# Kernel optimization log

Measured on AMD Instinct MI355X. Metric: run time of the kernel, lower is better.

Reference implementation:

```python
import jax, jax.numpy as jnp
import numpy as np
import math
from jax import lax

L = 16
T = 2 ** 14          # hash table size (power of 2 -> uint32 arithmetic is exact mod T)
F_DIM = 2
N_MIN, N_MAX = 16, 512
_B = math.exp((math.log(N_MAX) - math.log(N_MIN)) / (L - 1))
NS = [int(N_MIN * _B ** i) for i in range(L)]
PRIME = np.uint32(2654435761)


def setup_inputs() -> dict:
    key = jax.random.key(0)
    k1, k2 = jax.random.split(key)
    x = jax.random.uniform(k1, (8, 2, 512, 512), dtype=jnp.float32)
    hash_table = jax.random.uniform(k2, (L, T, F_DIM), dtype=jnp.float32) * 2e-4 - 1e-4
    return {"x": x, "hash_table": hash_table}


def reference(x, hash_table):
    b, c, h, w = x.shape
    feats = []
    for i, n in enumerate(NS):
        kh, kw = h // n, w // n
        # max_pool2d(x*n, (kh,kw), stride=1) -> [b, 2, h-kh+1, w-kw+1]
        g = lax.reduce_window(x * n, -jnp.inf, lax.max,
                              (1, 1, kh, kw), (1, 1, 1, 1), 'VALID')
        g = g.astype(jnp.uint32)  # trunc toward zero, values nonneg and small
        # prime-XOR hash; T is a power of two so uint32 wraparound matches int64 math mod T
        idx = (g[:, 0] ^ (g[:, 1] * PRIME)) % np.uint32(T)  # [b, gh, gw]
        f = hash_table[i][idx]                 # gather -> [b, gh, gw, F_DIM]
        f = jnp.transpose(f, (0, 3, 1, 2))     # [b, F_DIM, gh, gw]
        # bilinear upsample (half-pixel centers == align_corners=False)
        f = jax.image.resize(f, (b, F_DIM, h, w), method='bilinear')
        feats.append(f)
    return jnp.concatenate(feats, axis=1)       # [b, L*F_DIM, h, w]
```

## Files before the change

kernel.cpp:

```cpp
#include <hip/hip_runtime.h>
#include <stdint.h>

#define NLVL 16
#define TSIZE 16384
#define HW 512

typedef float vfloat4 __attribute__((ext_vector_type(4)));

__constant__ int c_n[NLVL] = {16,20,25,32,40,50,64,80,101,128,161,203,256,322,406,512};

__device__ __forceinline__ uint32_t pkmax(uint32_t a, uint32_t b) {
    uint32_t r;
    asm("v_pk_max_u16 %0, %1, %2" : "=v"(r) : "v"(a), "v"(b));
    return r;
}

template<int K>
__device__ __forceinline__ void do_tile(
        const int lvl, const int b, const int tx0, const int ty0,
        const float* __restrict__ x, const float* __restrict__ table,
        float* __restrict__ out, uint32_t* lds) {
    constexpr int gh = 513 - K;
    constexpr float s = (float)gh * (1.0f / 512.0f);
    const float nf = (float)c_n[lvl];
    const int tid = threadIdx.x;

    const float* xb0 = x + (size_t)b * 2 * HW * HW;
    const float* xb1 = xb0 + HW * HW;
    const float2* tb = (const float2*)table + (size_t)lvl * TSIZE;
    float* ob = out + ((size_t)b * 32 + lvl * 2) * HW * HW;

    if constexpr (K == 1) {
        const int oy = tid >> 3, xo = tx0 + (tid & 7) * 4;
        const int y = ty0 + oy;
        const float4 v0 = *(const float4*)&xb0[y * HW + xo];
        const float4 v1 = *(const float4*)&xb1[y * HW + xo];
        vfloat4 o0, o1;
        {
            const uint32_t i0 = (((uint32_t)(v0.x * nf)) ^ (((uint32_t)(v1.x * nf)) * 2654435761u)) & (TSIZE - 1);
            const uint32_t i1 = (((uint32_t)(v0.y * nf)) ^ (((uint32_t)(v1.y * nf)) * 2654435761u)) & (TSIZE - 1);
            const uint32_t i2 = (((uint32_t)(v0.z * nf)) ^ (((uint32_t)(v1.z * nf)) * 2654435761u)) & (TSIZE - 1);
            const uint32_t i3 = (((uint32_t)(v0.w * nf)) ^ (((uint32_t)(v1.w * nf)) * 2654435761u)) & (TSIZE - 1);
            const float2 f0 = tb[i0], f1 = tb[i1], f2 = tb[i2], f3 = tb[i3];
            o0 = (vfloat4){f0.x, f1.x, f2.x, f3.x};
            o1 = (vfloat4){f0.y, f1.y, f2.y, f3.y};
        }
        const size_t o = (size_t)y * HW + xo;
        __builtin_nontemporal_store(o0, (vfloat4*)&ob[o]);
        __builtin_nontemporal_store(o1, (vfloat4*)&ob[o + (size_t)HW * HW]);
        return;
    }

    uint32_t* V   = lds;
    float2*  feat = (float2*)(lds + 33 * 68);

    const int gy_base = (int)floorf(((float)ty0 + 0.5f) * s - 0.5f);
    const int gx_base = (int)floorf(((float)tx0 + 0.5f) * s - 0.5f);
    const int rmin = max(gy_base, 0);
    const int cmin = max(gx_base, 0);

    {
        const int wv = __builtin_amdgcn_readfirstlane(tid >> 6);
        const int c  = tid & 63;
        const int r0 = 8 * wv;
        const int xx = min(cmin + c, HW - 1);
        const int ybase = rmin + r0;
        uint32_t e[K + 8];
#pragma unroll
        for (int t = 0; t < K + 8; ++t) {
            const int yy = min(ybase + t, HW - 1);
            const float* rp0 = xb0 + yy * HW;
            const float* rp1 = xb1 + yy * HW;
            const float v0 = rp0[xx];
            const float v1 = rp1[xx];
            e[t] = (uint32_t)(v0 * nf) | ((uint32_t)(v1 * nf) << 16);
        }
        uint32_t o[9];
        if constexpr (K >= 10) {
            uint32_t sfx[9];
            sfx[8] = e[8];
#pragma unroll
            for (int t = 7; t >= 0; --t) sfx[t] = pkmax(e[t], sfx[t + 1]);
            uint32_t run = e[9];
#pragma unroll
            for (int m = 9; m <= K + 7; ++m) {
                if (m > 9) run = pkmax(run, e[m]);
                if (m >= K - 1) o[m - K + 1] = pkmax(sfx[m - K + 1], run);
            }
        } else {
#pragma unroll
            for (int i = 0; i < 9; ++i) {
                uint32_t m = e[i];
#pragma unroll
                for (int t = 1; t < K; ++t) m = pkmax(m, e[i + t]);
                o[i] = m;
            }
        }
        const int vb = r0 * 68 + c;
#pragma unroll
        for (int t = 0; t < 9; ++t) V[vb + t * 68] = o[t];
    }
    __syncthreads();

    if (tid < 99) {
        const int i = tid / 3, g = tid % 3;
        constexpr int NE  = 12 + K - 1;
        constexpr int NCH = (NE + 3) >> 2;
        uint32_t f[NCH * 4];
        const uint4* rp = (const uint4*)(V + i * 68 + 12 * g);
#pragma unroll
        for (int cc = 0; cc < NCH; ++cc) {
            const uint4 q = rp[cc];
            f[4*cc] = q.x; f[4*cc+1] = q.y; f[4*cc+2] = q.z; f[4*cc+3] = q.w;
        }
        uint32_t wm[12];
        if constexpr (K >= 13) {
            uint32_t sfx[12];
            sfx[11] = f[11];
#pragma unroll
            for (int d = 10; d >= 0; --d) sfx[d] = pkmax(f[d], sfx[d + 1]);
            uint32_t run = f[12];
#pragma unroll
            for (int m = 12; m <= K + 10; ++m) {
                if (m > 12) run = pkmax(run, f[m]);
                if (m >= K - 1) wm[m - K + 1] = pkmax(sfx[m - K + 1], run);
            }
        } else {
#pragma unroll
            for (int d = 0; d < 12; ++d) {
                uint32_t m = f[d];
#pragma unroll
                for (int t = 1; t < K; ++t) m = pkmax(m, f[d + t]);
                wm[d] = m;
            }
        }
#pragma unroll
        for (int d = 0; d < 12; ++d) {
            const int j = 12 * g + d;
            if (j < 33) {
                const uint32_t m = wm[d];
                const uint32_t idx = ((m & 0xFFFFu) ^ ((m >> 16) * 2654435761u)) & (TSIZE - 1);
                feat[i * 34 + j] = tb[idx];
            }
        }
    }
    __syncthreads();

    const int bty = tid >> 5, btx = tid & 31;
    const int xo = tx0 + btx;
    const float sxf = ((float)xo + 0.5f) * s - 0.5f;
    const float fxf = floorf(sxf);
    const float wx = sxf - fxf;
    const int x0i = (int)fxf;
    const int jx0 = min(max(x0i, 0), gh - 1) - cmin;
    const int jx1 = min(max(x0i + 1, 0), gh - 1) - cmin;
    for (int oy = bty; oy < 32; oy += 8) {
        const int y = ty0 + oy;
        const float syf = ((float)y + 0.5f) * s - 0.5f;
        const float fyf = floorf(syf);
        const float wy = syf - fyf;
        const int y0i = (int)fyf;
        const int iy0 = min(max(y0i, 0), gh - 1) - rmin;
        const int iy1 = min(max(y0i + 1, 0), gh - 1) - rmin;
        const float2 f00 = feat[iy0 * 34 + jx0], f01 = feat[iy0 * 34 + jx1];
        const float2 f10 = feat[iy1 * 34 + jx0], f11 = feat[iy1 * 34 + jx1];
        const float w11 = wy * wx;
        const float w10 = wy - w11;
        const float w01 = wx - w11;
        const float w00 = 1.0f - wy - wx + w11;
        const float c0 = f00.x * w00 + f01.x * w01 + f10.x * w10 + f11.x * w11;
        const float c1 = f00.y * w00 + f01.y * w01 + f10.y * w10 + f11.y * w11;
        const size_t o = (size_t)y * HW + xo;
        __builtin_nontemporal_store(c0, &ob[o]);
        __builtin_nontemporal_store(c1, &ob[o + (size_t)HW * HW]);
    }
}

__global__ __launch_bounds__(256) void fused_kernel(
        const float* __restrict__ x, const float* __restrict__ table,
        float* __restrict__ out) {
    __shared__ __align__(16) uint32_t lds[33 * 68 + 33 * 34 * 2];

    const int bid  = blockIdx.x;
    const int b    = bid & 7;
    const int tile = (bid >> 3) & 255;
    const int lvl  = bid >> 11;
    const int tx0  = (tile & 15) * 32;
    const int ty0  = (tile >> 4) * 32;

    switch (lvl) {
        case  0: do_tile<32>( 0, b, tx0, ty0, x, table, out, lds); break;
        case  1: do_tile<25>( 1, b, tx0, ty0, x, table, out, lds); break;
        case  2: do_tile<20>( 2, b, tx0, ty0, x, table, out, lds); break;
        case  3: do_tile<16>( 3, b, tx0, ty0, x, table, out, lds); break;
        case  4: do_tile<12>( 4, b, tx0, ty0, x, table, out, lds); break;
        case  5: do_tile<10>( 5, b, tx0, ty0, x, table, out, lds); break;
        case  6: do_tile< 8>( 6, b, tx0, ty0, x, table, out, lds); break;
        case  7: do_tile< 6>( 7, b, tx0, ty0, x, table, out, lds); break;
        case  8: do_tile< 5>( 8, b, tx0, ty0, x, table, out, lds); break;
        case  9: do_tile< 4>( 9, b, tx0, ty0, x, table, out, lds); break;
        case 10: do_tile< 3>(10, b, tx0, ty0, x, table, out, lds); break;
        case 11: do_tile< 2>(11, b, tx0, ty0, x, table, out, lds); break;
        case 12: do_tile< 2>(12, b, tx0, ty0, x, table, out, lds); break;
        case 13: do_tile< 1>(13, b, tx0, ty0, x, table, out, lds); break;
        case 14: do_tile< 1>(14, b, tx0, ty0, x, table, out, lds); break;
        default: do_tile< 1>(15, b, tx0, ty0, x, table, out, lds); break;
    }
}

extern "C" void kernel_launch(void* const* d_in, const int* in_sizes, int n_in,
                              void* d_out, int out_size, void* d_ws, size_t ws_size,
                              hipStream_t stream) {
    const float* x     = (const float*)d_in[0];
    const float* table = (const float*)d_in[1];
    float* out         = (float*)d_out;
    (void)d_ws; (void)ws_size;

    fused_kernel<<<dim3(NLVL * 256 * 8), dim3(256), 0, stream>>>(x, table, out);
}
```

Baseline: 111.3 us.

## Widen tiles to 64 columns with two-pixel-per-thread processing

Output tiles grow from 32x32 to 32x64, which halves the block count. Each thread now handles two adjacent columns: it reads x with float2 loads, runs packed max pooling on two columns, and writes two outputs per row with vector stores. The larger tile shrinks the relative halo overhead in the separable max-pool and gives wider memory transactions. In exchange it uses more LDS and registers per block, which can lower occupancy for the large-K levels, and there are half as many blocks to spread across the GPU.

```diff
diff --git a/kernel.cpp b/kernel.cpp
--- a/kernel.cpp
+++ b/kernel.cpp
@@ -6,6 +6,7 @@
 #define HW 512
 
 typedef float vfloat4 __attribute__((ext_vector_type(4)));
+typedef float vfloat2 __attribute__((ext_vector_type(2)));
 
 __constant__ int c_n[NLVL] = {16,20,25,32,40,50,64,80,101,128,161,203,256,322,406,512};
 
@@ -31,83 +32,89 @@
     float* ob = out + ((size_t)b * 32 + lvl * 2) * HW * HW;
 
     if constexpr (K == 1) {
-        const int oy = tid >> 3, xo = tx0 + (tid & 7) * 4;
-        const int y = ty0 + oy;
-        const float4 v0 = *(const float4*)&xb0[y * HW + xo];
-        const float4 v1 = *(const float4*)&xb1[y * HW + xo];
-        vfloat4 o0, o1;
-        {
+        const int r = tid >> 4, cq = tid & 15;
+        const int xo = tx0 + cq * 4;
+#pragma unroll
+        for (int it = 0; it < 2; ++it) {
+            const int y = ty0 + r + it * 16;
+            const float4 v0 = *(const float4*)&xb0[y * HW + xo];
+            const float4 v1 = *(const float4*)&xb1[y * HW + xo];
             const uint32_t i0 = (((uint32_t)(v0.x * nf)) ^ (((uint32_t)(v1.x * nf)) * 2654435761u)) & (TSIZE - 1);
             const uint32_t i1 = (((uint32_t)(v0.y * nf)) ^ (((uint32_t)(v1.y * nf)) * 2654435761u)) & (TSIZE - 1);
             const uint32_t i2 = (((uint32_t)(v0.z * nf)) ^ (((uint32_t)(v1.z * nf)) * 2654435761u)) & (TSIZE - 1);
             const uint32_t i3 = (((uint32_t)(v0.w * nf)) ^ (((uint32_t)(v1.w * nf)) * 2654435761u)) & (TSIZE - 1);
             const float2 f0 = tb[i0], f1 = tb[i1], f2 = tb[i2], f3 = tb[i3];
-            o0 = (vfloat4){f0.x, f1.x, f2.x, f3.x};
-            o1 = (vfloat4){f0.y, f1.y, f2.y, f3.y};
-        }
-        const size_t o = (size_t)y * HW + xo;
-        __builtin_nontemporal_store(o0, (vfloat4*)&ob[o]);
-        __builtin_nontemporal_store(o1, (vfloat4*)&ob[o + (size_t)HW * HW]);
+            const vfloat4 o0 = (vfloat4){f0.x, f1.x, f2.x, f3.x};
+            const vfloat4 o1 = (vfloat4){f0.y, f1.y, f2.y, f3.y};
+            const size_t o = (size_t)y * HW + xo;
+            __builtin_nontemporal_store(o0, (vfloat4*)&ob[o]);
+            __builtin_nontemporal_store(o1, (vfloat4*)&ob[o + (size_t)HW * HW]);
+        }
         return;
     }
 
     uint32_t* V   = lds;
-    float2*  feat = (float2*)(lds + 33 * 68);
+    float2*  feat = (float2*)(lds + 33 * 108);
 
     const int gy_base = (int)floorf(((float)ty0 + 0.5f) * s - 0.5f);
     const int gx_base = (int)floorf(((float)tx0 + 0.5f) * s - 0.5f);
-    const int rmin = max(gy_base, 0);
-    const int cmin = max(gx_base, 0);
-
+    const int rmin  = max(gy_base, 0);
+    const int cmin  = max(gx_base, 0);
+    const int xbase = cmin & ~1;
+
+    constexpr int NEEDC = 66 + K - 1;
+    constexpr int LANES = (NEEDC + 1) / 2;
     {
         const int wv = __builtin_amdgcn_readfirstlane(tid >> 6);
-        const int c  = tid & 63;
-        const int r0 = 8 * wv;
-        const int xx = min(cmin + c, HW - 1);
-        const int ybase = rmin + r0;
-        uint32_t e[K + 8];
-#pragma unroll
-        for (int t = 0; t < K + 8; ++t) {
-            const int yy = min(ybase + t, HW - 1);
-            const float* rp0 = xb0 + yy * HW;
-            const float* rp1 = xb1 + yy * HW;
-            const float v0 = rp0[xx];
-            const float v1 = rp1[xx];
-            e[t] = (uint32_t)(v0 * nf) | ((uint32_t)(v1 * nf) << 16);
-        }
-        uint32_t o[9];
-        if constexpr (K >= 10) {
-            uint32_t sfx[9];
-            sfx[8] = e[8];
-#pragma unroll
-            for (int t = 7; t >= 0; --t) sfx[t] = pkmax(e[t], sfx[t + 1]);
-            uint32_t run = e[9];
-#pragma unroll
-            for (int m = 9; m <= K + 7; ++m) {
-                if (m > 9) run = pkmax(run, e[m]);
-                if (m >= K - 1) o[m - K + 1] = pkmax(sfx[m - K + 1], run);
-            }
-        } else {
-#pragma unroll
-            for (int i = 0; i < 9; ++i) {
-                uint32_t m = e[i];
-#pragma unroll
-                for (int t = 1; t < K; ++t) m = pkmax(m, e[i + t]);
-                o[i] = m;
-            }
-        }
-        const int vb = r0 * 68 + c;
-#pragma unroll
-        for (int t = 0; t < 9; ++t) V[vb + t * 68] = o[t];
+        const int l  = tid & 63;
+        if (l < LANES) {
+            const int r0 = 8 * wv;
+            const int xx = min(xbase + 2 * l, HW - 2);
+            const int ybase = rmin + r0;
+            uint32_t eA[K + 8], eB[K + 8];
+#pragma unroll
+            for (int t = 0; t < K + 8; ++t) {
+                const int yy = min(ybase + t, HW - 1);
+                const float2 v0 = *(const float2*)(xb0 + yy * HW + xx);
+                const float2 v1 = *(const float2*)(xb1 + yy * HW + xx);
+                eA[t] = (uint32_t)(v0.x * nf) | ((uint32_t)(v1.x * nf) << 16);
+                eB[t] = (uint32_t)(v0.y * nf) | ((uint32_t)(v1.y * nf) << 16);
+            }
+            uint32_t oA[9], oB[9];
+            if constexpr (K >= 10) {
+                uint32_t sA[9], sB[9];
+                sA[8] = eA[8]; sB[8] = eB[8];
+#pragma unroll
+                for (int t = 7; t >= 0; --t) { sA[t] = pkmax(eA[t], sA[t+1]); sB[t] = pkmax(eB[t], sB[t+1]); }
+                uint32_t rA = eA[9], rB = eB[9];
+#pragma unroll
+                for (int m = 9; m <= K + 7; ++m) {
+                    if (m > 9) { rA = pkmax(rA, eA[m]); rB = pkmax(rB, eB[m]); }
+                    if (m >= K - 1) { oA[m-K+1] = pkmax(sA[m-K+1], rA); oB[m-K+1] = pkmax(sB[m-K+1], rB); }
+                }
+            } else {
+#pragma unroll
+                for (int i = 0; i < 9; ++i) {
+                    uint32_t mA = eA[i], mB = eB[i];
+#pragma unroll
+                    for (int t = 1; t < K; ++t) { mA = pkmax(mA, eA[i+t]); mB = pkmax(mB, eB[i+t]); }
+                    oA[i] = mA; oB[i] = mB;
+                }
+            }
+            const int vb = r0 * 108 + 2 * l;
+#pragma unroll
+            for (int t = 0; t < 9; ++t)
+                *(uint2*)(V + vb + t * 108) = make_uint2(oA[t], oB[t]);
+        }
     }
     __syncthreads();
 
-    if (tid < 99) {
-        const int i = tid / 3, g = tid % 3;
+    if (tid < 198) {
+        const int i = tid / 6, g = tid % 6;
         constexpr int NE  = 12 + K - 1;
         constexpr int NCH = (NE + 3) >> 2;
         uint32_t f[NCH * 4];
-        const uint4* rp = (const uint4*)(V + i * 68 + 12 * g);
+        const uint4* rp = (const uint4*)(V + i * 108 + 12 * g);
 #pragma unroll
         for (int cc = 0; cc < NCH; ++cc) {
             const uint4 q = rp[cc];
@@ -136,24 +143,30 @@
         }
 #pragma unroll
         for (int d = 0; d < 12; ++d) {
-            const int j = 12 * g + d;
-            if (j < 33) {
+            const int p = 12 * g + d;
+            if (p < 66) {
                 const uint32_t m = wm[d];
                 const uint32_t idx = ((m & 0xFFFFu) ^ ((m >> 16) * 2654435761u)) & (TSIZE - 1);
-                feat[i * 34 + j] = tb[idx];
+                feat[i * 68 + p] = tb[idx];
             }
         }
     }
     __syncthreads();
 
     const int bty = tid >> 5, btx = tid & 31;
-    const int xo = tx0 + btx;
-    const float sxf = ((float)xo + 0.5f) * s - 0.5f;
-    const float fxf = floorf(sxf);
-    const float wx = sxf - fxf;
-    const int x0i = (int)fxf;
-    const int jx0 = min(max(x0i, 0), gh - 1) - cmin;
-    const int jx1 = min(max(x0i + 1, 0), gh - 1) - cmin;
+    const int xo = tx0 + 2 * btx;
+    const float sxA = ((float)xo + 0.5f) * s - 0.5f;
+    const float fxA = floorf(sxA);
+    const float wxA = sxA - fxA;
+    const int xiA = (int)fxA;
+    const int jA0 = min(max(xiA, 0), gh - 1) - xbase;
+    const int jA1 = min(max(xiA + 1, 0), gh - 1) - xbase;
+    const float sxB = ((float)xo + 1.5f) * s - 0.5f;
+    const float fxB = floorf(sxB);
+    const float wxB = sxB - fxB;
+    const int xiB = (int)fxB;
+    const int jB0 = min(max(xiB, 0), gh - 1) - xbase;
+    const int jB1 = min(max(xiB + 1, 0), gh - 1) - xbase;
     for (int oy = bty; oy < 32; oy += 8) {
         const int y = ty0 + oy;
         const float syf = ((float)y + 0.5f) * s - 0.5f;
@@ -162,31 +175,33 @@
         const int y0i = (int)fyf;
         const int iy0 = min(max(y0i, 0), gh - 1) - rmin;
         const int iy1 = min(max(y0i + 1, 0), gh - 1) - rmin;
-        const float2 f00 = feat[iy0 * 34 + jx0], f01 = feat[iy0 * 34 + jx1];
-        const float2 f10 = feat[iy1 * 34 + jx0], f11 = feat[iy1 * 34 + jx1];
-        const float w11 = wy * wx;
-        const float w10 = wy - w11;
-        const float w01 = wx - w11;
-        const float w00 = 1.0f - wy - wx + w11;
-        const float c0 = f00.x * w00 + f01.x * w01 + f10.x * w10 + f11.x * w11;
-        const float c1 = f00.y * w00 + f01.y * w01 + f10.y * w10 + f11.y * w11;
+        const float2* r0f = feat + iy0 * 68;
+        const float2* r1f = feat + iy1 * 68;
+        const float2 a00 = r0f[jA0], a01 = r0f[jA1], a10 = r1f[jA0], a11 = r1f[jA1];
+        const float wA11 = wy * wxA, wA10 = wy - wA11, wA01 = wxA - wA11, wA00 = 1.0f - wy - wxA + wA11;
+        const float cA0 = a00.x * wA00 + a01.x * wA01 + a10.x * wA10 + a11.x * wA11;
+        const float cA1 = a00.y * wA00 + a01.y * wA01 + a10.y * wA10 + a11.y * wA11;
+        const float2 b00 = r0f[jB0], b01 = r0f[jB1], b10 = r1f[jB0], b11 = r1f[jB1];
+        const float wB11 = wy * wxB, wB10 = wy - wB11, wB01 = wxB - wB11, wB00 = 1.0f - wy - wxB + wB11;
+        const float cB0 = b00.x * wB00 + b01.x * wB01 + b10.x * wB10 + b11.x * wB11;
+        const float cB1 = b00.y * wB00 + b01.y * wB01 + b10.y * wB10 + b11.y * wB11;
         const size_t o = (size_t)y * HW + xo;
-        __builtin_nontemporal_store(c0, &ob[o]);
-        __builtin_nontemporal_store(c1, &ob[o + (size_t)HW * HW]);
+        __builtin_nontemporal_store((vfloat2){cA0, cB0}, (vfloat2*)&ob[o]);
+        __builtin_nontemporal_store((vfloat2){cA1, cB1}, (vfloat2*)&ob[o + (size_t)HW * HW]);
     }
 }
 
 __global__ __launch_bounds__(256) void fused_kernel(
         const float* __restrict__ x, const float* __restrict__ table,
         float* __restrict__ out) {
-    __shared__ __align__(16) uint32_t lds[33 * 68 + 33 * 34 * 2];
+    __shared__ __align__(16) uint32_t lds[33 * 108 + 33 * 68 * 2];
 
     const int bid  = blockIdx.x;
     const int b    = bid & 7;
-    const int tile = (bid >> 3) & 255;
-    const int lvl  = bid >> 11;
-    const int tx0  = (tile & 15) * 32;
-    const int ty0  = (tile >> 4) * 32;
+    const int tile = (bid >> 3) & 127;
+    const int lvl  = bid >> 10;
+    const int tx0  = (tile & 7) * 64;
+    const int ty0  = (tile >> 3) * 32;
 
     switch (lvl) {
         case  0: do_tile<32>( 0, b, tx0, ty0, x, table, out, lds); break;
@@ -216,5 +231,5 @@
     float* out         = (float*)d_out;
     (void)d_ws; (void)ws_size;
 
-    fused_kernel<<<dim3(NLVL * 256 * 8), dim3(256), 0, stream>>>(x, table, out);
-}
+    fused_kernel<<<dim3(NLVL * 128 * 8), dim3(256), 0, stream>>>(x, table, out);
+}
```

After: 123.1 us. +10.6%, slower.
